# Kernel tuning notes

Hardware: AMD Instinct MI355X
Metric: run time of the kernel (lower is better)

Reference implementation:

```python
import jax, jax.numpy as jnp
import numpy as np

EPS = 1e-8  # matches torch F.cosine_similarity eps default


def setup_inputs() -> dict:
    key = jax.random.key(0)
    k1, k2 = jax.random.split(key)
    z = jax.random.normal(k1, (8192, 256), dtype=jnp.float32)            # [N, d] node latents
    embedding_weight = jax.random.normal(k2, (4096, 256), dtype=jnp.float32)  # [V, d] codebook
    return {"z": z, "embedding_weight": embedding_weight}


def _l2_normalize(x):
    # torch cosine_similarity clamps each norm at eps before dividing
    n = jnp.sqrt(jnp.sum(x * x, axis=-1, keepdims=True))
    return x / jnp.maximum(n, EPS)


def reference(z, embedding_weight):
    # decode_edges: sigmoid(z @ z^T) -> [N, N]
    adj = jax.nn.sigmoid(jnp.matmul(z, z.T))

    # decode_node_features: cosine similarity of every node latent vs every
    # codebook vector, then argmax over the codebook axis. Instead of the
    # naive [N, V, d] broadcast, normalize both sides and take a single
    # [N, d] x [d, V] matmul -> [N, V], then reduce with argmax.
    zn = _l2_normalize(z)                   # [N, d]
    en = _l2_normalize(embedding_weight)    # [V, d]
    cosine_sim = jnp.matmul(zn, en.T)       # [N, V]
    decoded_indices = jnp.argmax(cosine_sim, axis=1)  # [N] int

    return adj, decoded_indices
```

## Files before the change

### kernel.cpp

```cpp
#include <hip/hip_runtime.h>
#include <stdint.h>
#include <math.h>

#define D_DIM 256
#define NZ 8192
#define NV 4096
#define CAP 128
#define THR_C 0.138f
#define MARGIN 0.012f

typedef __bf16 bf16;
typedef __attribute__((ext_vector_type(8))) __bf16 bf16x8;
typedef __attribute__((ext_vector_type(4))) float f32x4;

__device__ __forceinline__ void stage16(const bf16* g, bf16* lbase) {
#if __has_builtin(__builtin_amdgcn_global_load_lds)
  __builtin_amdgcn_global_load_lds(
      (const __attribute__((address_space(1))) void*)(uintptr_t)g,
      (__attribute__((address_space(3))) void*)(uint32_t)(uintptr_t)lbase,
      16, 0, 0);
#endif
}

__global__ void prep_kernel(const float* __restrict__ z, const float* __restrict__ E,
                            bf16* __restrict__ zh, bf16* __restrict__ zl,
                            bf16* __restrict__ eh, float* __restrict__ rinvZ,
                            float* __restrict__ rinvE,
                            unsigned long long* __restrict__ slots,
                            unsigned int* __restrict__ cnt) {
  __shared__ float red[4];
  const int row = blockIdx.x;
  const int t = threadIdx.x;
  const bool isZ = row < NZ;
  const int r = isZ ? row : row - NZ;
  const float* src = isZ ? z : E;
  const float x = src[(size_t)r * D_DIM + t];
  const bf16 h = (bf16)x;
  if (isZ) {
    zh[(size_t)r * D_DIM + t] = h;
    zl[(size_t)r * D_DIM + t] = (bf16)(x - (float)h);
  } else {
    eh[(size_t)r * D_DIM + t] = h;
  }
  float s = x * x;
#pragma unroll
  for (int off = 32; off; off >>= 1) s += __shfl_xor(s, off);
  if ((t & 63) == 0) red[t >> 6] = s;
  __syncthreads();
  if (t == 0) {
    const float tot = red[0] + red[1] + red[2] + red[3];
    const float rv = 1.0f / fmaxf(sqrtf(tot), 1e-8f);
    if (isZ) {
      rinvZ[r] = rv;
      slots[r] = 0ull;
      cnt[r] = 0u;
    } else {
      rinvE[r] = rv;
    }
  }
}

__device__ __forceinline__ unsigned long long packvc(float v, int col) {
  const uint32_t b = __float_as_uint(v);
  const uint32_t key = b ^ ((uint32_t)((int32_t)b >> 31) | 0x80000000u);
  return ((unsigned long long)key << 32) | (uint32_t)(~(uint32_t)col);
}
__device__ __forceinline__ float unpack_v(unsigned long long p) {
  const uint32_t key = (uint32_t)(p >> 32);
  const uint32_t fb = (key & 0x80000000u) ? (key ^ 0x80000000u) : ~key;
  return __uint_as_float(fb);
}
__device__ __forceinline__ int unpack_c(unsigned long long p) {
  return (int)(~(uint32_t)p);
}

__global__ __launch_bounds__(256, 3) void cos_kernel(
    const bf16* __restrict__ Ah, const bf16* __restrict__ Bh,
    const float* __restrict__ rinvZ, const float* __restrict__ rinvE,
    unsigned long long* __restrict__ slots, unsigned long long* __restrict__ cand,
    unsigned int* __restrict__ cnt) {
  __shared__ bf16 lAh[128 * 32], lBh[128 * 32];
  const int tid = threadIdx.x;
  const int lane = tid & 63;
  const int w = tid >> 6;
  const int wr = w >> 1, wc = w & 1;
  const int l15 = lane & 15, q = lane >> 4;
  const int bm = blockIdx.y * 128;
  const int bn = blockIdx.x * 128;

  f32x4 acc[4][4] = {};

  for (int kt = 0; kt < 8; ++kt) {
    const int ko = kt * 32;
#pragma unroll
    for (int i = 0; i < 2; ++i) {
      const int c = w * 128 + i * 64 + lane;
      const int r = c >> 2;
      const int kb = (c & 3) << 3;
      const int lofs = (w * 128 + i * 64) * 8;
      stage16(Ah + (size_t)(bm + r) * D_DIM + ko + kb, lAh + lofs);
      stage16(Bh + (size_t)(bn + r) * D_DIM + ko + kb, lBh + lofs);
    }
    __syncthreads();
    bf16x8 fb[4];
#pragma unroll
    for (int ns = 0; ns < 4; ++ns)
      fb[ns] = *(const bf16x8*)&lBh[(wc * 64 + ns * 16 + l15) * 32 + q * 8];
#pragma unroll
    for (int ms = 0; ms < 4; ++ms) {
      const bf16x8 fa = *(const bf16x8*)&lAh[(wr * 64 + ms * 16 + l15) * 32 + q * 8];
#pragma unroll
      for (int ns = 0; ns < 4; ++ns)
        acc[ms][ns] = __builtin_amdgcn_mfma_f32_16x16x32_bf16(fa, fb[ns], acc[ms][ns], 0, 0, 0);
    }
    __syncthreads();
  }

  float rc[4];
  int cols[4];
#pragma unroll
  for (int ns = 0; ns < 4; ++ns) {
    cols[ns] = bn + wc * 64 + ns * 16 + l15;
    rc[ns] = rinvE[cols[ns]];
  }
#pragma unroll
  for (int ms = 0; ms < 4; ++ms) {
    const int rb = bm + wr * 64 + ms * 16 + q * 4;
#pragma unroll
    for (int r = 0; r < 4; ++r) {
      const int rowg = rb + r;
      const float rr = rinvZ[rowg];
      unsigned long long best = 0ull;
#pragma unroll
      for (int ns = 0; ns < 4; ++ns) {
        const float v = acc[ms][ns][r] * rc[ns] * rr;
        const unsigned long long p = packvc(v, cols[ns]);
        best = p > best ? p : best;
        if (v >= THR_C) {
          const unsigned int k = atomicAdd(&cnt[rowg], 1u);
          if (k < CAP) cand[(size_t)rowg * CAP + k] = p;
        }
      }
#pragma unroll
      for (int off = 1; off < 16; off <<= 1) {
        const unsigned long long o = __shfl_xor(best, off);
        best = o > best ? o : best;
      }
      if (l15 == 0) atomicMax(&slots[rowg], best);
    }
  }
}

__device__ __forceinline__ int tri_base(int i) { return i * 64 - ((i * (i - 1)) >> 1); }

__global__ __launch_bounds__(256, 3) void adj_kernel(const bf16* __restrict__ Ah,
                                                     const bf16* __restrict__ Al,
                                                     float* __restrict__ out) {
  __shared__ bf16 lAh[128 * 32], lAl[128 * 32], lBh[128 * 32], lBl[128 * 32];
  int k = blockIdx.x;
  k = (k & 7) * 260 + (k >> 3);
  const double disc = 4160.25 - 2.0 * (double)k;
  int bi = (int)(64.5 - sqrt(disc));
  while (tri_base(bi + 1) <= k) ++bi;
  while (tri_base(bi) > k) --bi;
  const int bj = bi + (k - tri_base(bi));
  const int bm = bi * 128, bn = bj * 128;

  const int tid = threadIdx.x;
  const int lane = tid & 63;
  const int w = tid >> 6;
  const int wr = w >> 1, wc = w & 1;
  const int l15 = lane & 15, q = lane >> 4;

  f32x4 acc[4][4] = {};

  for (int kt = 0; kt < 8; ++kt) {
    const int ko = kt * 32;
#pragma unroll
    for (int i = 0; i < 2; ++i) {
      const int c = w * 128 + i * 64 + lane;
      const int r = c >> 2;
      const int kb = (c & 3) << 3;
      const size_t ga = (size_t)(bm + r) * D_DIM + ko + kb;
      const size_t gb = (size_t)(bn + r) * D_DIM + ko + kb;
      const int lofs = (w * 128 + i * 64) * 8;
      stage16(Ah + ga, lAh + lofs);
      stage16(Al + ga, lAl + lofs);
      stage16(Ah + gb, lBh + lofs);
      stage16(Al + gb, lBl + lofs);
    }
    __syncthreads();
    bf16x8 fbh[4], fbl[4];
#pragma unroll
    for (int ns = 0; ns < 4; ++ns) {
      const int n = wc * 64 + ns * 16 + l15;
      fbh[ns] = *(const bf16x8*)&lBh[n * 32 + q * 8];
      fbl[ns] = *(const bf16x8*)&lBl[n * 32 + q * 8];
    }
#pragma unroll
    for (int ms = 0; ms < 4; ++ms) {
      const int m = wr * 64 + ms * 16 + l15;
      const bf16x8 fah = *(const bf16x8*)&lAh[m * 32 + q * 8];
      const bf16x8 fal = *(const bf16x8*)&lAl[m * 32 + q * 8];
#pragma unroll
      for (int ns = 0; ns < 4; ++ns) {
        acc[ms][ns] = __builtin_amdgcn_mfma_f32_16x16x32_bf16(fah, fbh[ns], acc[ms][ns], 0, 0, 0);
        acc[ms][ns] = __builtin_amdgcn_mfma_f32_16x16x32_bf16(fah, fbl[ns], acc[ms][ns], 0, 0, 0);
        acc[ms][ns] = __builtin_amdgcn_mfma_f32_16x16x32_bf16(fal, fbh[ns], acc[ms][ns], 0, 0, 0);
      }
    }
    __syncthreads();
  }

#pragma unroll
  for (int ms = 0; ms < 4; ++ms)
#pragma unroll
    for (int ns = 0; ns < 4; ++ns)
#pragma unroll
      for (int r = 0; r < 4; ++r)
        acc[ms][ns][r] = __builtin_amdgcn_rcpf(1.0f + __expf(-acc[ms][ns][r]));

#pragma unroll
  for (int ms = 0; ms < 4; ++ms) {
    const int rb = bm + wr * 64 + ms * 16 + q * 4;
#pragma unroll
    for (int r = 0; r < 4; ++r) {
      const size_t ro = (size_t)(rb + r) * NZ;
#pragma unroll
      for (int ns = 0; ns < 4; ++ns) {
        const int col = bn + wc * 64 + ns * 16 + l15;
        out[ro + col] = acc[ms][ns][r];
      }
    }
  }
  if (bi != bj) {
#pragma unroll
    for (int ms = 0; ms < 4; ++ms) {
      const int rb = bm + wr * 64 + ms * 16 + q * 4;
#pragma unroll
      for (int ns = 0; ns < 4; ++ns) {
        const int col = bn + wc * 64 + ns * 16 + l15;
        *(f32x4*)&out[(size_t)col * NZ + rb] = acc[ms][ns];
      }
    }
  }
}

__global__ __launch_bounds__(256) void refine_kernel(
    const unsigned long long* __restrict__ cand, const unsigned int* __restrict__ cnt,
    const unsigned long long* __restrict__ slots, const float* __restrict__ z,
    const float* __restrict__ E, float* __restrict__ out_idx) {
  const int t = threadIdx.x;
  const int lane = t & 63;
  const int w = t >> 6;
  const int row = blockIdx.x * 4 + w;

  const int n = (int)min(cnt[row], (unsigned int)CAP);

  if (n == 0) {
    if (lane == 0) out_idx[row] = (float)unpack_c(slots[row]);
    return;
  }

  double zr[4];
#pragma unroll
  for (int j = 0; j < 4; ++j) zr[j] = (double)z[(size_t)row * D_DIM + lane + 64 * j];
  double sz2 = zr[0] * zr[0] + zr[1] * zr[1] + zr[2] * zr[2] + zr[3] * zr[3];
#pragma unroll
  for (int off = 32; off; off >>= 1) sz2 += __shfl_xor(sz2, off);
  const double sz = fmax(sqrt(sz2), 1e-8);

  const unsigned long long* lrow = cand + (size_t)row * CAP;
  unsigned long long mk = 0ull;
  for (int i = lane; i < n; i += 64) {
    const unsigned long long p = lrow[i];
    mk = p > mk ? p : mk;
  }
#pragma unroll
  for (int off = 32; off; off >>= 1) {
    const unsigned long long o = __shfl_xor(mk, off);
    mk = o > mk ? o : mk;
  }
  const float thr = unpack_v(mk) - MARGIN;

  double v1 = -1e30, v2 = -1e30;
  int c1 = 0x7fffffff, c2 = 0x7fffffff;
  for (int i = 0; i < n; ++i) {
    const unsigned long long p = lrow[i];
    if (unpack_v(p) < thr) continue;
    const int c = unpack_c(p);
    double d = 0.0, e2 = 0.0;
#pragma unroll
    for (int j = 0; j < 4; ++j) {
      const double ev = (double)E[(size_t)c * D_DIM + lane + 64 * j];
      d += zr[j] * ev;
      e2 += ev * ev;
    }
#pragma unroll
    for (int off = 32; off; off >>= 1) {
      d += __shfl_xor(d, off);
      e2 += __shfl_xor(e2, off);
    }
    const double cv = d / (sz * fmax(sqrt(e2), 1e-8));
    if (cv > v1 || (cv == v1 && c < c1)) {
      v2 = v1; c2 = c1; v1 = cv; c1 = c;
    } else if (cv > v2 || (cv == v2 && c < c2)) {
      v2 = cv; c2 = c;
    }
  }
  if (lane == 0) {
    int pick = c1;
    if (c2 != 0x7fffffff && (v1 - v2) < 3e-7) pick = c2;
    out_idx[row] = (float)pick;
  }
}

extern "C" void kernel_launch(void* const* d_in, const int* in_sizes, int n_in,
                              void* d_out, int out_size, void* d_ws, size_t ws_size,
                              hipStream_t stream) {
  const float* z = (const float*)d_in[0];
  const float* E = (const float*)d_in[1];
  float* out = (float*)d_out;

  char* ws = (char*)d_ws;
  bf16* zh = (bf16*)ws;
  bf16* zl = zh + (size_t)NZ * D_DIM;
  bf16* eh = zl + (size_t)NZ * D_DIM;
  float* rinvZ = (float*)(eh + (size_t)NV * D_DIM);
  float* rinvE = rinvZ + NZ;
  unsigned long long* slots = (unsigned long long*)(rinvE + NV);

  unsigned long long* cand = (unsigned long long*)out;
  unsigned int* cnt = (unsigned int*)(cand + (size_t)NZ * CAP);
  float* idx_out = out + (size_t)NZ * NZ;

  prep_kernel<<<NZ + NV, 256, 0, stream>>>(z, E, zh, zl, eh, rinvZ, rinvE, slots, cnt);

  dim3 g2(NV / 128, NZ / 128);
  cos_kernel<<<g2, 256, 0, stream>>>(zh, eh, rinvZ, rinvE, slots, cand, cnt);

  refine_kernel<<<NZ / 4, 256, 0, stream>>>(cand, cnt, slots, z, E, idx_out);

  adj_kernel<<<2080, 256, 0, stream>>>(zh, zl, out);
}
```

Measured before the change: 460.0 us.

## Replace capped candidate list with per-bucket atomicMax candidate table

The per-row candidate list, which used an atomic counter and a 128-entry cap, is replaced by 256 fixed buckets per row. Each bucket covers 16 codebook columns and keeps only its best packed value through atomicMax. This removes the contended counter atomics and the overflow risk from the cap. The refine kernel now reads the whole bucket table and uses a ballot so it runs the double-precision dot product only on flagged buckets. In exchange, prep must zero a larger table, and when two close candidates share a bucket only the best one survives.

```diff
diff --git a/kernel.cpp b/kernel.cpp
--- a/kernel.cpp
+++ b/kernel.cpp
@@ -5,7 +5,7 @@
 #define D_DIM 256
 #define NZ 8192
 #define NV 4096
-#define CAP 128
+#define NBKT 256
 #define THR_C 0.138f
 #define MARGIN 0.012f
 
@@ -27,7 +27,7 @@
                             bf16* __restrict__ eh, float* __restrict__ rinvZ,
                             float* __restrict__ rinvE,
                             unsigned long long* __restrict__ slots,
-                            unsigned int* __restrict__ cnt) {
+                            unsigned long long* __restrict__ cand) {
   __shared__ float red[4];
   const int row = blockIdx.x;
   const int t = threadIdx.x;
@@ -39,6 +39,7 @@
   if (isZ) {
     zh[(size_t)r * D_DIM + t] = h;
     zl[(size_t)r * D_DIM + t] = (bf16)(x - (float)h);
+    cand[(size_t)r * NBKT + t] = 0ull;
   } else {
     eh[(size_t)r * D_DIM + t] = h;
   }
@@ -53,7 +54,6 @@
     if (isZ) {
       rinvZ[r] = rv;
       slots[r] = 0ull;
-      cnt[r] = 0u;
     } else {
       rinvE[r] = rv;
     }
@@ -77,8 +77,7 @@
 __global__ __launch_bounds__(256, 3) void cos_kernel(
     const bf16* __restrict__ Ah, const bf16* __restrict__ Bh,
     const float* __restrict__ rinvZ, const float* __restrict__ rinvE,
-    unsigned long long* __restrict__ slots, unsigned long long* __restrict__ cand,
-    unsigned int* __restrict__ cnt) {
+    unsigned long long* __restrict__ slots, unsigned long long* __restrict__ cand) {
   __shared__ bf16 lAh[128 * 32], lBh[128 * 32];
   const int tid = threadIdx.x;
   const int lane = tid & 63;
@@ -137,8 +136,7 @@
         const unsigned long long p = packvc(v, cols[ns]);
         best = p > best ? p : best;
         if (v >= THR_C) {
-          const unsigned int k = atomicAdd(&cnt[rowg], 1u);
-          if (k < CAP) cand[(size_t)rowg * CAP + k] = p;
+          atomicMax(&cand[(size_t)rowg * NBKT + (cols[ns] >> 4)], p);
         }
       }
 #pragma unroll
@@ -247,7 +245,7 @@
 }
 
 __global__ __launch_bounds__(256) void refine_kernel(
-    const unsigned long long* __restrict__ cand, const unsigned int* __restrict__ cnt,
+    const unsigned long long* __restrict__ cand,
     const unsigned long long* __restrict__ slots, const float* __restrict__ z,
     const float* __restrict__ E, float* __restrict__ out_idx) {
   const int t = threadIdx.x;
@@ -255,57 +253,61 @@
   const int w = t >> 6;
   const int row = blockIdx.x * 4 + w;
 
-  const int n = (int)min(cnt[row], (unsigned int)CAP);
-
-  if (n == 0) {
-    if (lane == 0) out_idx[row] = (float)unpack_c(slots[row]);
-    return;
-  }
-
-  double zr[4];
-#pragma unroll
-  for (int j = 0; j < 4; ++j) zr[j] = (double)z[(size_t)row * D_DIM + lane + 64 * j];
-  double sz2 = zr[0] * zr[0] + zr[1] * zr[1] + zr[2] * zr[2] + zr[3] * zr[3];
-#pragma unroll
-  for (int off = 32; off; off >>= 1) sz2 += __shfl_xor(sz2, off);
-  const double sz = fmax(sqrt(sz2), 1e-8);
-
-  const unsigned long long* lrow = cand + (size_t)row * CAP;
+  const unsigned long long* lrow = cand + (size_t)row * NBKT;
+  unsigned long long pj[4];
   unsigned long long mk = 0ull;
-  for (int i = lane; i < n; i += 64) {
-    const unsigned long long p = lrow[i];
-    mk = p > mk ? p : mk;
+#pragma unroll
+  for (int j = 0; j < 4; ++j) {
+    pj[j] = lrow[lane + 64 * j];
+    mk = pj[j] > mk ? pj[j] : mk;
   }
 #pragma unroll
   for (int off = 32; off; off >>= 1) {
     const unsigned long long o = __shfl_xor(mk, off);
     mk = o > mk ? o : mk;
   }
+  if (mk == 0ull) {
+    if (lane == 0) out_idx[row] = (float)unpack_c(slots[row]);
+    return;
+  }
   const float thr = unpack_v(mk) - MARGIN;
+
+  double zr[4];
+#pragma unroll
+  for (int j = 0; j < 4; ++j) zr[j] = (double)z[(size_t)row * D_DIM + lane + 64 * j];
+  double sz2 = zr[0] * zr[0] + zr[1] * zr[1] + zr[2] * zr[2] + zr[3] * zr[3];
+#pragma unroll
+  for (int off = 32; off; off >>= 1) sz2 += __shfl_xor(sz2, off);
+  const double sz = fmax(sqrt(sz2), 1e-8);
 
   double v1 = -1e30, v2 = -1e30;
   int c1 = 0x7fffffff, c2 = 0x7fffffff;
-  for (int i = 0; i < n; ++i) {
-    const unsigned long long p = lrow[i];
-    if (unpack_v(p) < thr) continue;
-    const int c = unpack_c(p);
-    double d = 0.0, e2 = 0.0;
-#pragma unroll
-    for (int j = 0; j < 4; ++j) {
-      const double ev = (double)E[(size_t)c * D_DIM + lane + 64 * j];
-      d += zr[j] * ev;
-      e2 += ev * ev;
-    }
-#pragma unroll
-    for (int off = 32; off; off >>= 1) {
-      d += __shfl_xor(d, off);
-      e2 += __shfl_xor(e2, off);
-    }
-    const double cv = d / (sz * fmax(sqrt(e2), 1e-8));
-    if (cv > v1 || (cv == v1 && c < c1)) {
-      v2 = v1; c2 = c1; v1 = cv; c1 = c;
-    } else if (cv > v2 || (cv == v2 && c < c2)) {
-      v2 = cv; c2 = c;
+#pragma unroll
+  for (int j = 0; j < 4; ++j) {
+    const bool flag = (pj[j] != 0ull) && (unpack_v(pj[j]) >= thr);
+    unsigned long long bal = __ballot(flag);
+    while (bal) {
+      const int src = __ffsll((long long)bal) - 1;
+      bal &= bal - 1;
+      const int c = unpack_c(__shfl(pj[j], src));
+      double d = 0.0, e2 = 0.0;
+#pragma unroll
+      for (int jj = 0; jj < 4; ++jj) {
+        const double ev = (double)E[(size_t)c * D_DIM + lane + 64 * jj];
+        d += zr[jj] * ev;
+        e2 += ev * ev;
+      }
+#pragma unroll
+      for (int off = 32; off; off >>= 1) {
+        d += __shfl_xor(d, off);
+        e2 += __shfl_xor(e2, off);
+      }
+      const double cv = d / (sz * fmax(sqrt(e2), 1e-8));
+      if (cv > v1 || (cv == v1 && c < c1)) {
+        v2 = v1; c2 = c1; v1 = cv; c1 = c;
+      } else if (cv > v2 || (cv == v2 && c < c2)) {
+        v2 = cv; c2 = c;
+      }
     }
   }
   if (lane == 0) {
@@ -331,15 +333,14 @@
   unsigned long long* slots = (unsigned long long*)(rinvE + NV);
 
   unsigned long long* cand = (unsigned long long*)out;
-  unsigned int* cnt = (unsigned int*)(cand + (size_t)NZ * CAP);
   float* idx_out = out + (size_t)NZ * NZ;
 
-  prep_kernel<<<NZ + NV, 256, 0, stream>>>(z, E, zh, zl, eh, rinvZ, rinvE, slots, cnt);
+  prep_kernel<<<NZ + NV, 256, 0, stream>>>(z, E, zh, zl, eh, rinvZ, rinvE, slots, cand);
 
   dim3 g2(NV / 128, NZ / 128);
-  cos_kernel<<<g2, 256, 0, stream>>>(zh, eh, rinvZ, rinvE, slots, cand, cnt);
-
-  refine_kernel<<<NZ / 4, 256, 0, stream>>>(cand, cnt, slots, z, E, idx_out);
+  cos_kernel<<<g2, 256, 0, stream>>>(zh, eh, rinvZ, rinvE, slots, cand);
+
+  refine_kernel<<<NZ / 4, 256, 0, stream>>>(cand, slots, z, E, idx_out);
 
   adj_kernel<<<2080, 256, 0, stream>>>(zh, zl, out);
 }
```

New measurement: 406.8 us. 1.13x faster.
